# Optimization experiments

Hardware: AMD Instinct MI355X
Metric: run time of the kernel (lower is better)

## Reference

```python
import jax, jax.numpy as jnp
import numpy as np
from jax import lax

B, H, W = 2, 960, 1280
K = 1024            # max_keypoints
P = 256             # num_pairs (BAD descriptor dim)
NUM_SCALES = 3
DIFF_ITERS = 3
KAPPA = 0.05
TAU = 0.2           # explicit FED step size (stable < 0.25)
DET_THRESHOLD = 0.001
AKAZE_NMS = 5       # detector-internal NMS window
NMS_WIN = 2 * 3 + 1 # pipeline NMS window (nms_radius=3)
ORI_PATCH = 15
ORI_SIGMA = 2.5
SINK_ITERS = 20
EPSILON = 1.0
UNUSED_SCORE = 1.0
MAX_RADIUS = 5

def _conv(x, k):
    return lax.conv_general_dilated(x, k, (1, 1), 'SAME', dimension_numbers=('NCHW', 'OIHW', 'NCHW'))

_sob = np.array([[-1., 0., 1.], [-2., 0., 2.], [-1., 0., 1.]], np.float32) / 8.0
KX = jnp.asarray(_sob)[None, None]
KY = jnp.asarray(_sob.T)[None, None]
_d2 = np.array([[0., 0., 0.], [1., -2., 1.], [0., 0., 0.]], np.float32)
KXX = jnp.asarray(_d2)[None, None]
KYY = jnp.asarray(_d2.T)[None, None]

# Gaussian weighting kernel for orientation estimation
_c = np.arange(ORI_PATCH, dtype=np.float32) - (ORI_PATCH - 1) / 2.0
_gy, _gx = np.meshgrid(_c, _c, indexing='ij')
_g = np.exp(-(_gx ** 2 + _gy ** 2) / (2.0 * ORI_SIGMA ** 2))
GK = jnp.asarray((_g / _g.sum()).astype(np.float32))[None, None]

# Box-average kernel bank: one normalized box filter per radius 0..MAX_RADIUS
_bc = np.arange(-MAX_RADIUS, MAX_RADIUS + 1, dtype=np.float32)
_by, _bx = np.meshgrid(_bc, _bc, indexing='ij')
_rv = np.arange(MAX_RADIUS + 1, dtype=np.float32)[:, None, None]
_bm = ((np.abs(_by) <= _rv) & (np.abs(_bx) <= _rv)).astype(np.float32)
BOX_BANK = jnp.asarray((_bm / (2.0 * _rv + 1.0) ** 2)[:, None])  # [R+1,1,11,11]

def _shifts(a):
    p = jnp.pad(a, ((0, 0), (0, 0), (1, 1), (1, 1)), mode='edge')
    return p[:, :, :-2, 1:-1], p[:, :, 2:, 1:-1], p[:, :, 1:-1, :-2], p[:, :, 1:-1, 2:]

def _fed_step(L):
    # One explicit Perona-Malik (FED) nonlinear diffusion step
    Lx = _conv(L, KX); Ly = _conv(L, KY)
    g = 1.0 / (1.0 + (Lx * Lx + Ly * Ly) / (KAPPA * KAPPA))
    Ln, Ls, Lw, Le = _shifts(L)
    gn, gs, gw, ge = _shifts(g)
    flux = 0.5 * ((g + gn) * (Ln - L) + (g + gs) * (Ls - L) + (g + gw) * (Lw - L) + (g + ge) * (Le - L))
    return L + TAU * flux

def _maxpool(s, win):
    return lax.reduce_window(s, -jnp.inf, lax.max, (1, win, win), (1, 1, 1), 'SAME')

def _akaze(img):
    # Multi-scale FED diffusion -> Hessian determinant response + orientation map
    L = img
    resp = jnp.zeros((B, H, W), img.dtype)
    for _s in range(NUM_SCALES):
        for _i in range(DIFF_ITERS):
            L = _fed_step(L)
        Lxx = _conv(L, KXX); Lyy = _conv(L, KYY); Lxy = _conv(_conv(L, KX), KY)
        resp = jnp.maximum(resp, (Lxx * Lyy - Lxy * Lxy)[:, 0])
    resp = jnp.where(resp > DET_THRESHOLD, resp, 0.0)
    resp = resp * (resp >= _maxpool(resp, AKAZE_NMS) - 1e-7).astype(resp.dtype)
    gxs = _conv(_conv(img, KX), GK)[:, 0]
    gys = _conv(_conv(img, KY), GK)[:, 0]
    theta = jnp.arctan2(gys, gxs)  # [B,H,W]
    return resp, theta

def _select(resp):
    # Pipeline-level maxpool NMS + top-K selection, pad invalid with (-1,-1)
    mask = (resp >= _maxpool(resp, NMS_WIN) - 1e-7).astype(resp.dtype)
    s = resp * mask
    s = jnp.where(s > 0.0, s, 0.0)
    tk, idx = lax.top_k(s.reshape(B, -1), K)
    y = (idx // W).astype(jnp.float32)
    x = (idx % W).astype(jnp.float32)
    valid = (tk > 0.0).astype(jnp.float32)
    kpts = jnp.where(valid[..., None] > 0.5, jnp.stack([y, x], -1), -1.0)
    return kpts, tk * valid, valid

def _bad(img, kpts, theta, valid, offsets, radii, thresholds):
    # Orientation-aware BAD: box-averaged intensity differences at rotated pair offsets
    bank = _conv(img, BOX_BANK)  # [B,R+1,H,W]
    yc = jnp.clip(kpts[..., 0], 0.0, H - 1.0)
    xc = jnp.clip(kpts[..., 1], 0.0, W - 1.0)
    yi = jnp.round(yc).astype(jnp.int32); xi = jnp.round(xc).astype(jnp.int32)
    th = jax.vmap(lambda m, a, b: m[a, b])(theta, yi, xi)  # [B,K] nearest-sampled orientation
    c = jnp.cos(th)[..., None]; s = jnp.sin(th)[..., None]
    ox1, oy1, ox2, oy2 = offsets[:, 0], offsets[:, 1], offsets[:, 2], offsets[:, 3]
    px1 = xc[..., None] + c * ox1 - s * oy1
    py1 = yc[..., None] + s * ox1 + c * oy1
    px2 = xc[..., None] + c * ox2 - s * oy2
    py2 = yc[..., None] + s * ox2 + c * oy2
    rb = jnp.broadcast_to(radii[None, :], (K, P))
    def samp(px, py):
        xi_ = jnp.clip(jnp.round(px), 0, W - 1).astype(jnp.int32)
        yi_ = jnp.clip(jnp.round(py), 0, H - 1).astype(jnp.int32)
        return jax.vmap(lambda bk, a, b: bk[rb, a, b])(bank, yi_, xi_)  # [B,K,P]
    v = (samp(px1, py1) - samp(px2, py2)) - thresholds[None, None, :]
    v = v * valid[..., None]
    n = jnp.linalg.norm(v, axis=-1, keepdims=True)
    return v / (n + 1e-8)

def _sinkhorn(d1, d2):
    sq1 = jnp.sum(d1 * d1, -1); sq2 = jnp.sum(d2 * d2, -1)
    dist2 = sq1[:, :, None] + sq2[:, None, :] - 2.0 * jnp.einsum('bip,bjp->bij', d1, d2)
    dist = jnp.sqrt(jnp.maximum(dist2, 0.0) + 1e-12)
    Z = jnp.full((B, K + 1, K + 1), UNUSED_SCORE, d1.dtype)
    Z = Z.at[:, :K, :K].set(-dist) / EPSILON
    norm = -jnp.log(2.0 * K)
    log_mu = jnp.concatenate([jnp.zeros(K, Z.dtype), jnp.log(float(K)) * jnp.ones(1, Z.dtype)]) + norm
    log_nu = log_mu
    def body(carry, _):
        u, v = carry
        u = log_mu[None] - jax.nn.logsumexp(Z + v[:, None, :], axis=2)
        v = log_nu[None] - jax.nn.logsumexp(Z + u[:, :, None], axis=1)
        return (u, v), None
    (u, v), _ = lax.scan(body, (jnp.zeros((B, K + 1), Z.dtype), jnp.zeros((B, K + 1), Z.dtype)), None, length=SINK_ITERS)
    return jnp.exp(Z + u[:, :, None] + v[:, None, :] - norm)  # [B,K+1,K+1]

def _forward(img1, img2, offsets, thresholds, radii):
    r1, t1 = _akaze(img1)
    r2, t2 = _akaze(img2)
    k1, s1, v1 = _select(r1)
    k2, s2, v2 = _select(r2)
    d1 = _bad(img1, k1, t1, v1, offsets, radii, thresholds)
    d2 = _bad(img2, k2, t2, v2, offsets, radii, thresholds)
    probs = _sinkhorn(d1, d2)
    return k1, k2, probs

def setup_inputs():
    key = jax.random.key(0)
    k1, k2, k3, k4, k5 = jax.random.split(key, 5)
    img1 = jax.random.uniform(k1, (B, 1, H, W), jnp.float32)
    img2 = jax.random.uniform(k2, (B, 1, H, W), jnp.float32)
    offsets = jax.random.uniform(k3, (P, 4), jnp.float32, -16.0, 16.0)  # box_params - 16
    thresholds = 0.05 * jax.random.normal(k5, (P,), jnp.float32)
    radii = jax.random.randint(k4, (P,), 0, MAX_RADIUS + 1, jnp.int32)
    return {'img1': img1, 'img2': img2, 'offsets': offsets, 'thresholds': thresholds, 'radii': radii}

def reference(img1, img2, offsets, thresholds, radii):
    return _forward(img1, img2, offsets, thresholds, radii)
```

## Files before the change

kernel.cpp:

```cpp
#include <hip/hip_runtime.h>
#include <hip/hip_fp16.h>
#include <math.h>

typedef unsigned long long u64;
typedef unsigned int u32;

#define Hh 960
#define Ww 1280
#define Bb 2
#define Kk 1024
#define Pp 256
#define KP1 1025
#define NSEG 4
#define LISTCAP 131072
#define PR 28
#define PS 57
#define ZLD 1040
static const size_t ZB = (size_t)KP1*ZLD;

static const size_t HWp = (size_t)Hh * Ww;
static const size_t PLn = HWp * Bb;

#define TAUf 0.2f
#define NMS_EPS 1e-7f
#define DET_T 0.001f
#define NORMV (-7.6246189861593985f)
#define LOGKV (6.9314718055994531f)

__constant__ float WR[6] = {1.0f, 1.0f/9.0f, 1.0f/25.0f, 1.0f/49.0f, 1.0f/81.0f, 1.0f/121.0f};

__device__ __forceinline__ int imin(int a,int b){return a<b?a:b;}
__device__ __forceinline__ int imax(int a,int b){return a>b?a:b;}

__global__ __launch_bounds__(256) void fed_step(const float* __restrict__ src, float* __restrict__ dst){
  __shared__ float Lt[36][37];
  __shared__ float Gt[34][35];
  const int bx = blockIdx.x*32, by = blockIdx.y*32, b = blockIdx.z;
  const float* S = src + (size_t)b*HWp;
  float* D = dst + (size_t)b*HWp;
  const int t = threadIdx.y*32 + threadIdx.x;
  for (int i=t;i<36*36;i+=256){
    int ly=i/36, lx=i-ly*36;
    int gy=by+ly-2, gx=bx+lx-2;
    Lt[ly][lx] = (gy>=0 && gy<Hh && gx>=0 && gx<Ww) ? S[(size_t)gy*Ww+gx] : 0.0f;
  }
  __syncthreads();
  const float k2 = (float)(0.05*0.05);
  for (int i=t;i<34*34;i+=256){
    int ly=i/34, lx=i-ly*34;
    int Ly=ly+1, Lx=lx+1;
    float sx = (-Lt[Ly-1][Lx-1]+Lt[Ly-1][Lx+1]
                -2.0f*Lt[Ly][Lx-1]+2.0f*Lt[Ly][Lx+1]
                -Lt[Ly+1][Lx-1]+Lt[Ly+1][Lx+1])*0.125f;
    float sy = (-Lt[Ly-1][Lx-1]-2.0f*Lt[Ly-1][Lx]-Lt[Ly-1][Lx+1]
                +Lt[Ly+1][Lx-1]+2.0f*Lt[Ly+1][Lx]+Lt[Ly+1][Lx+1])*0.125f;
    Gt[ly][lx] = 1.0f/(1.0f + (sx*sx+sy*sy)/k2);
  }
  __syncthreads();
  for (int r=0;r<4;++r){
    int oy=threadIdx.y + r*8, ox=threadIdx.x;
    int gy=by+oy, gx=bx+ox;
    if (gy>=Hh || gx>=Ww) continue;
    int gyn=imax(gy-1,0), gys=imin(gy+1,Hh-1), gxw=imax(gx-1,0), gxe=imin(gx+1,Ww-1);
    float Lc=Lt[oy+2][ox+2];
    float Ln=Lt[gyn-by+2][ox+2];
    float Ls=Lt[gys-by+2][ox+2];
    float Lw=Lt[oy+2][gxw-bx+2];
    float Le=Lt[oy+2][gxe-bx+2];
    float gc=Gt[oy+1][ox+1];
    float gn=Gt[gyn-by+1][ox+1];
    float gs=Gt[gys-by+1][ox+1];
    float gw=Gt[oy+1][gxw-bx+1];
    float ge=Gt[oy+1][gxe-bx+1];
    float flux = 0.5f*((gc+gn)*(Ln-Lc) + (gc+gs)*(Ls-Lc) + (gc+gw)*(Lw-Lc) + (gc+ge)*(Le-Lc));
    D[(size_t)gy*Ww+gx] = Lc + TAUf*flux;
  }
}

__global__ __launch_bounds__(256) void response_kernel(const float* __restrict__ src, float* __restrict__ resp, int first){
  __shared__ float Lt[36][37];
  __shared__ float Sx[34][35];
  const int bx = blockIdx.x*32, by = blockIdx.y*32, b = blockIdx.z;
  const float* S = src + (size_t)b*HWp;
  float* R = resp + (size_t)b*HWp;
  const int t = threadIdx.y*32 + threadIdx.x;
  for (int i=t;i<36*36;i+=256){
    int ly=i/36, lx=i-ly*36;
    int gy=by+ly-2, gx=bx+lx-2;
    Lt[ly][lx] = (gy>=0 && gy<Hh && gx>=0 && gx<Ww) ? S[(size_t)gy*Ww+gx] : 0.0f;
  }
  __syncthreads();
  for (int i=t;i<34*34;i+=256){
    int ly=i/34, lx=i-ly*34;
    int gy=by+ly-1, gx=bx+lx-1;
    float v=0.0f;
    if (gy>=0 && gy<Hh && gx>=0 && gx<Ww){
      int Ly=ly+1, Lx=lx+1;
      v = (-Lt[Ly-1][Lx-1]+Lt[Ly-1][Lx+1]
           -2.0f*Lt[Ly][Lx-1]+2.0f*Lt[Ly][Lx+1]
           -Lt[Ly+1][Lx-1]+Lt[Ly+1][Lx+1])*0.125f;
    }
    Sx[ly][lx]=v;
  }
  __syncthreads();
  for (int r=0;r<4;++r){
    int oy=threadIdx.y + r*8, ox=threadIdx.x;
    int gy=by+oy, gx=bx+ox;
    if (gy>=Hh || gx>=Ww) continue;
    int Ly=oy+2, Lx=ox+2;
    float Lxx = Lt[Ly][Lx-1]-2.0f*Lt[Ly][Lx]+Lt[Ly][Lx+1];
    float Lyy = Lt[Ly-1][Lx]-2.0f*Lt[Ly][Lx]+Lt[Ly+1][Lx];
    int Sy=oy+1, Sxi=ox+1;
    float Lxy = (-Sx[Sy-1][Sxi-1]-2.0f*Sx[Sy-1][Sxi]-Sx[Sy-1][Sxi+1]
                 +Sx[Sy+1][Sxi-1]+2.0f*Sx[Sy+1][Sxi]+Sx[Sy+1][Sxi+1])*0.125f;
    float det = Lxx*Lyy - Lxy*Lxy;
    size_t id=(size_t)gy*Ww+gx;
    R[id] = first ? fmaxf(det,0.0f) : fmaxf(R[id], det);
  }
}

__global__ __launch_bounds__(256) void detect_compact(const float* __restrict__ resp,
                                                      u64* __restrict__ lists,
                                                      int* __restrict__ cnt, int segbase){
  const int TS=42;
  __shared__ float Tt[TS][TS+1];
  __shared__ float H5[TS][40];
  __shared__ float Ss[38][39];
  __shared__ u64 keys[1024];
  __shared__ int lcnt, gbase;
  const int bx = blockIdx.x*32, by = blockIdx.y*32, b = blockIdx.z;
  const float* S = resp + (size_t)b*HWp;
  const int t = threadIdx.y*32 + threadIdx.x;
  if (t==0) lcnt=0;
  for (int i=t;i<TS*TS;i+=256){
    int ly=i/TS, lx=i-ly*TS;
    int gy=by+ly-5, gx=bx+lx-5;
    float v = (gy>=0 && gy<Hh && gx>=0 && gx<Ww) ? S[(size_t)gy*Ww+gx] : 0.0f;
    Tt[ly][lx] = (v>DET_T) ? v : 0.0f;
  }
  __syncthreads();
  for (int i=t;i<42*38;i+=256){
    int y=i/38, x=i-(i/38)*38;
    float m=Tt[y][x];
    m=fmaxf(m,Tt[y][x+1]); m=fmaxf(m,Tt[y][x+2]);
    m=fmaxf(m,Tt[y][x+3]); m=fmaxf(m,Tt[y][x+4]);
    H5[y][x]=m;
  }
  __syncthreads();
  for (int i=t;i<38*38;i+=256){
    int y=i/38, x=i-(i/38)*38;
    float m=H5[y][x];
    m=fmaxf(m,H5[y+1][x]); m=fmaxf(m,H5[y+2][x]);
    m=fmaxf(m,H5[y+3][x]); m=fmaxf(m,H5[y+4][x]);
    float c=Tt[y+2][x+2];
    Ss[y][x]=(c>=m-NMS_EPS)?c:0.0f;
  }
  __syncthreads();
  const int seg=segbase+b;
  for (int r=0;r<4;++r){
    int oy=threadIdx.y + r*8, ox=threadIdx.x;
    int gy=by+oy, gx=bx+ox;
    bool pos=false; u64 key=0;
    if (gy<Hh && gx<Ww){
      float v=Ss[oy+3][ox+3];
      if (v>0.0f){
        float m=0.0f;
        #pragma unroll
        for(int dy=0;dy<7;dy++)
          #pragma unroll
          for(int dx=0;dx<7;dx++)
            m=fmaxf(m,Ss[oy+dy][ox+dx]);
        if (v>=m-NMS_EPS){
          u32 idx=(u32)(gy*Ww+gx);
          key=((u64)__float_as_uint(v)<<32)|(u64)(0xFFFFFFFFu-idx);
          pos=true;
        }
      }
    }
    u64 mask=__ballot(pos);
    if (mask){
      int lane=t&63;
      int leader=__ffsll((long long)mask)-1;
      int base=0;
      if (lane==leader) base=atomicAdd(&lcnt,__popcll(mask));
      base=__shfl(base,leader);
      if (pos){
        int rk=__popcll(mask & ((1ULL<<lane)-1ULL));
        keys[base+rk]=key;
      }
    }
  }
  __syncthreads();
  if (t==0 && lcnt>0) gbase=atomicAdd(&cnt[seg*64], lcnt);
  __syncthreads();
  int n=lcnt;
  for (int i=t;i<n;i+=256){
    int p=gbase+i;
    if (p<LISTCAP) lists[(size_t)seg*LISTCAP+p]=keys[i];
  }
}

__global__ __launch_bounds__(1024) void topk_one(const u64* __restrict__ lists, const int* __restrict__ cnt,
                                                 u64* __restrict__ selbuf, int* __restrict__ selcnt){
  const int seg=blockIdx.x, tid=threadIdx.x;
  __shared__ u32 h[256];
  __shared__ u32 scan[256];
  __shared__ int krem_s, ta_s, bsel, lbase;
  __shared__ u64 pfx_s;
  const int n=imin(cnt[seg*64],LISTCAP);
  const u64* L=lists+(size_t)seg*LISTCAP;
  if(tid==0){ krem_s=Kk; pfx_s=0ULL; ta_s=(n<=Kk)?1:0; lbase=0; }
  __syncthreads();
  u64 T=1ULL;
  if(!ta_s){
    for(int rd=0;rd<8;rd++){
      int shift=56-8*rd;
      u64 maskHi=(rd==0)?0ULL:(~0ULL<<(shift+8));
      u64 pfx=pfx_s;
      if(tid<256) h[tid]=0;
      __syncthreads();
      for(int i=tid;i<n;i+=1024){
        u64 k=L[i];
        if((k&maskHi)==pfx) atomicAdd(&h[(int)((k>>shift)&255ULL)],1u);
      }
      __syncthreads();
      if(tid<256) scan[tid]=h[tid];
      __syncthreads();
      for(int off=1;off<256;off<<=1){
        u32 v=0;
        if(tid<256 && tid+off<256) v=scan[tid+off];
        __syncthreads();
        if(tid<256) scan[tid]+=v;
        __syncthreads();
      }
      int kr=krem_s;
      if(tid<256){
        bool ge=(scan[tid]>=(u32)kr);
        bool geN=(tid<255)?(scan[tid+1]>=(u32)kr):false;
        if(ge && !geN) bsel=tid;
      }
      __syncthreads();
      if(tid==0){
        int b=bsel;
        int acc=(b<255)?(int)scan[b+1]:0;
        pfx_s |= ((u64)(u32)b)<<shift;
        krem_s = kr-acc;
      }
      __syncthreads();
    }
    T=pfx_s;
  }
  __syncthreads();
  for(int i0=0;i0<n;i0+=1024){
    int i=i0+tid;
    bool sel=false; u64 k=0;
    if(i<n){ k=L[i]; sel=(k>=T); }
    u64 mask=__ballot(sel);
    if(mask){
      int lane=tid&63;
      int leader=__ffsll((long long)mask)-1;
      int base=0;
      if(lane==leader) base=atomicAdd(&lbase,__popcll(mask));
      base=__shfl(base,leader);
      if(sel){
        int p=base+__popcll(mask & ((1ULL<<lane)-1ULL));
        if(p<Kk) selbuf[(size_t)seg*Kk+p]=k;
      }
    }
  }
  __syncthreads();
  if(tid==0) selcnt[seg*64]=imin(lbase,Kk);
}

__global__ __launch_bounds__(1024) void finalize_kernel(const u64* __restrict__ selbuf, const int* __restrict__ selcnt,
                                int* __restrict__ kyi, int* __restrict__ kxi, float* __restrict__ kval,
                                float* __restrict__ outp){
  int seg=blockIdx.x, tid=threadIdx.x;
  __shared__ u64 a[1024];
  int n=selcnt[seg*64]; if(n>Kk)n=Kk;
  a[tid]=(tid<n)?selbuf[(size_t)seg*Kk+tid]:0ULL;
  __syncthreads();
  for(int k=2;k<=1024;k<<=1){
    for(int j=k>>1;j>0;j>>=1){
      int ixj=tid^j;
      if(ixj>tid){
        u64 x=a[tid], y=a[ixj];
        bool desc=((tid&k)==0);
        if(desc ? (x<y) : (x>y)){ a[tid]=y; a[ixj]=x; }
      }
      __syncthreads();
    }
  }
  u64 key=a[tid];
  bool val=(key!=0ULL);
  u32 idx=0xFFFFFFFFu-(u32)(key&0xFFFFFFFFULL);
  int y= val ? (int)(idx/Ww) : 0;
  int x= val ? (int)(idx%Ww) : 0;
  int mi=seg*Kk+tid;
  kyi[mi]=y; kxi[mi]=x; kval[mi]= val?1.0f:0.0f;
  int imi=seg>>1, bb=seg&1;
  float* ko=outp + (size_t)imi*(Bb*Kk*2) + ((size_t)bb*Kk+tid)*2;
  ko[0]= val ? (float)y : -1.0f;
  ko[1]= val ? (float)x : -1.0f;
}

__global__ void init_weights(float* wn){
  if(threadIdx.x==0 && blockIdx.x==0){
    double w[15]; double S=0.0;
    for(int i=0;i<15;i++){ double c=(double)i-7.0; w[i]=exp(-(c*c)/(2.0*2.5*2.5)); S+=w[i]; }
    for(int i=0;i<15;i++) wn[i]=(float)(w[i]/S);
  }
}

__device__ __forceinline__ float ldz(const float* __restrict__ img,int y,int x){
  return (y>=0&&y<Hh&&x>=0&&x<Ww)?img[(size_t)y*Ww+x]:0.0f;
}

__global__ __launch_bounds__(64) void orient_kernel(const float* __restrict__ img1, const float* __restrict__ img2,
                              const int* __restrict__ kyi, const int* __restrict__ kxi,
                              const float* __restrict__ wn, float* __restrict__ kth){
  int seg=blockIdx.y, ki=blockIdx.x, lane=threadIdx.x;
  __shared__ float w15[15];
  if(lane<15) w15[lane]=wn[lane];
  __syncthreads();
  const float* img=(seg<2?img1:img2)+(size_t)(seg&1)*HWp;
  int mi=seg*Kk+ki;
  int yc=kyi[mi], xc=kxi[mi];
  float ax=0.0f, ay=0.0f;
  for(int tp=lane;tp<225;tp+=64){
    int du=tp/15-7, dv=tp-(tp/15)*15-7;
    int yy=yc+du, xx=xc+dv;
    if(yy<0||yy>=Hh||xx<0||xx>=Ww) continue;
    float p00=ldz(img,yy-1,xx-1), p01=ldz(img,yy-1,xx), p02=ldz(img,yy-1,xx+1);
    float p10=ldz(img,yy,xx-1),                          p12=ldz(img,yy,xx+1);
    float p20=ldz(img,yy+1,xx-1), p21=ldz(img,yy+1,xx), p22=ldz(img,yy+1,xx+1);
    float sx=(-p00+p02-2.0f*p10+2.0f*p12-p20+p22)*0.125f;
    float sy=(-p00-2.0f*p01-p02+p20+2.0f*p21+p22)*0.125f;
    float wgt=w15[du+7]*w15[dv+7];
    ax=fmaf(wgt,sx,ax); ay=fmaf(wgt,sy,ay);
  }
  for(int o=32;o;o>>=1){ ax+=__shfl_down(ax,o); ay+=__shfl_down(ay,o); }
  if(lane==0) kth[mi]=atan2f(ay,ax);
}

__global__ __launch_bounds__(256) void bad_kernel(const float* __restrict__ img1, const float* __restrict__ img2,
                           const float* __restrict__ offs, const float* __restrict__ thrv,
                           const int* __restrict__ rad,
                           const int* __restrict__ kyi, const int* __restrict__ kxi,
                           const float* __restrict__ kval, const float* __restrict__ kth,
                           float* __restrict__ d1, float* __restrict__ d2,
                           float* __restrict__ sq1, float* __restrict__ sq2){
  __shared__ float sat[PS+1][PS+2];
  __shared__ float sm[4];
  __shared__ float nsh;
  int seg=blockIdx.y, ki=blockIdx.x, p=threadIdx.x;
  const float* img=(seg<2?img1:img2)+(size_t)(seg&1)*HWp;
  int mi=seg*Kk+ki;
  int yci=kyi[mi], xci=kxi[mi];
  for (int i=p;i<PS+1;i+=256){ sat[0][i]=0.0f; sat[i][0]=0.0f; }
  if (p==0) sat[0][PS]=0.0f;
  for (int i=p;i<PS*PS;i+=256){
    int ly=i/PS, lx=i-ly*PS;
    int gy=yci-PR+ly, gx=xci-PR+lx;
    sat[ly+1][lx+1]=(gy>=0&&gy<Hh&&gx>=0&&gx<Ww)?img[(size_t)gy*Ww+gx]:0.0f;
  }
  __syncthreads();
  if (p<PS){
    float run=0.0f;
    for(int x=1;x<=PS;x++){ run+=sat[p+1][x]; sat[p+1][x]=run; }
  }
  __syncthreads();
  if (p<PS){
    float run=0.0f;
    for(int y=1;y<=PS;y++){ run+=sat[y][p+1]; sat[y][p+1]=run; }
  }
  __syncthreads();
  float yc=(float)yci, xc=(float)xci;
  float th=kth[mi];
  float c=cosf(th), s=sinf(th);
  float ox1=offs[p*4+0], oy1=offs[p*4+1], ox2=offs[p*4+2], oy2=offs[p*4+3];
  int r=rad[p];
  float w=WR[r];
  float px1=xc+c*ox1-s*oy1, py1=yc+s*ox1+c*oy1;
  float px2=xc+c*ox2-s*oy2, py2=yc+s*ox2+c*oy2;
  auto boxl=[&](float px,float py,int r_)->float{
    float rx=rintf(px), ry=rintf(py);
    int xi=(int)fminf(fmaxf(rx,0.0f),(float)(Ww-1));
    int yi=(int)fminf(fmaxf(ry,0.0f),(float)(Hh-1));
    int lx=xi-(xci-PR), ly=yi-(yci-PR);
    int y2=ly+r_+1, y1=ly-r_, x2=lx+r_+1, x1=lx-r_;
    return sat[y2][x2]-sat[y1][x2]-sat[y2][x1]+sat[y1][x1];
  };
  float s1=boxl(px1,py1,r)*w;
  float s2=boxl(px2,py2,r)*w;
  float v=(s1-s2-thrv[p])*kval[mi];
  float t=v*v;
  for(int o=32;o;o>>=1) t+=__shfl_down(t,o);
  if((p&63)==0) sm[p>>6]=t;
  __syncthreads();
  if(p==0) nsh=sqrtf(sm[0]+sm[1]+sm[2]+sm[3]);
  __syncthreads();
  float dv=v/(nsh+1e-8f);
  float* dd=(seg<2?d1:d2);
  dd[((size_t)(seg&1)*Kk+ki)*Pp+p]=dv;
  float t2=dv*dv;
  for(int o=32;o;o>>=1) t2+=__shfl_down(t2,o);
  __syncthreads();
  if((p&63)==0) sm[p>>6]=t2;
  __syncthreads();
  if(p==0){ float* sq=(seg<2?sq1:sq2); sq[(size_t)(seg&1)*Kk+ki]=sm[0]+sm[1]+sm[2]+sm[3]; }
}

__global__ __launch_bounds__(256) void dist_kernel(const float* __restrict__ d1, const float* __restrict__ d2,
                            const float* __restrict__ sq1, const float* __restrict__ sq2,
                            float* __restrict__ Zm, float* __restrict__ Zt){
  int b=blockIdx.z;
  int i0=blockIdx.y*64, j0=blockIdx.x*64;
  int tid=threadIdx.x;
  int tx=tid&15, ty=tid>>4;
  __shared__ float Ast[64][68], Bst[64][68];
  const float* D1=d1+(size_t)b*Kk*Pp;
  const float* D2=d2+(size_t)b*Kk*Pp;
  float acc[4][4]={};
  for(int p0=0;p0<Pp;p0+=64){
    for(int i=tid;i<64*16;i+=256){
      int row=i>>4, c4=(i&15)<<2;
      float4 va=*reinterpret_cast<const float4*>(&D1[(size_t)(i0+row)*Pp+p0+c4]);
      float4 vb=*reinterpret_cast<const float4*>(&D2[(size_t)(j0+row)*Pp+p0+c4]);
      Ast[c4+0][row]=va.x; Ast[c4+1][row]=va.y; Ast[c4+2][row]=va.z; Ast[c4+3][row]=va.w;
      Bst[c4+0][row]=vb.x; Bst[c4+1][row]=vb.y; Bst[c4+2][row]=vb.z; Bst[c4+3][row]=vb.w;
    }
    __syncthreads();
    #pragma unroll 8
    for(int kk=0;kk<64;++kk){
      float4 av=*reinterpret_cast<const float4*>(&Ast[kk][ty*4]);
      float4 bv=*reinterpret_cast<const float4*>(&Bst[kk][tx*4]);
      acc[0][0]=fmaf(av.x,bv.x,acc[0][0]); acc[0][1]=fmaf(av.x,bv.y,acc[0][1]);
      acc[0][2]=fmaf(av.x,bv.z,acc[0][2]); acc[0][3]=fmaf(av.x,bv.w,acc[0][3]);
      acc[1][0]=fmaf(av.y,bv.x,acc[1][0]); acc[1][1]=fmaf(av.y,bv.y,acc[1][1]);
      acc[1][2]=fmaf(av.y,bv.z,acc[1][2]); acc[1][3]=fmaf(av.y,bv.w,acc[1][3]);
      acc[2][0]=fmaf(av.z,bv.x,acc[2][0]); acc[2][1]=fmaf(av.z,bv.y,acc[2][1]);
      acc[2][2]=fmaf(av.z,bv.z,acc[2][2]); acc[2][3]=fmaf(av.z,bv.w,acc[2][3]);
      acc[3][0]=fmaf(av.w,bv.x,acc[3][0]); acc[3][1]=fmaf(av.w,bv.y,acc[3][1]);
      acc[3][2]=fmaf(av.w,bv.z,acc[3][2]); acc[3][3]=fmaf(av.w,bv.w,acc[3][3]);
    }
    __syncthreads();
  }
  int gi=i0+ty*4, gj=j0+tx*4;
  float si[4], sj[4];
  #pragma unroll
  for(int i=0;i<4;i++){ si[i]=sq1[b*Kk+gi+i]; sj[i]=sq2[b*Kk+gj+i]; }
  #pragma unroll
  for(int i=0;i<4;i++){
    #pragma unroll
    for(int j=0;j<4;j++){
      float dd=si[i]+sj[j]-2.0f*acc[i][j];
      float dist=sqrtf(fmaxf(dd,0.0f)+1e-12f);
      Zm[(size_t)b*ZB+(size_t)(gi+i)*ZLD+(gj+j)]=-dist;
      Zt[(size_t)b*ZB+(size_t)(gj+j)*ZLD+(gi+i)]=-dist;
    }
  }
}

__global__ void zborder_kernel(float* __restrict__ Zm, float* __restrict__ Zt){
  int i=blockIdx.x*256+threadIdx.x;
  if(i>=Bb*KP1) return;
  int b=i/KP1, j=i-(i/KP1)*KP1;
  size_t base=(size_t)b*ZB;
  Zm[base+(size_t)j*ZLD+Kk]=1.0f;
  Zm[base+(size_t)Kk*ZLD+j]=1.0f;
  Zt[base+(size_t)j*ZLD+Kk]=1.0f;
  Zt[base+(size_t)Kk*ZLD+j]=1.0f;
  for(int c=KP1;c<ZLD;c++){
    Zm[base+(size_t)j*ZLD+c]=-1.0e30f;
    Zt[base+(size_t)j*ZLD+c]=-1.0e30f;
  }
}

__global__ void expz_kernel(const float* __restrict__ Zm, const float* __restrict__ Zt,
                            __half* __restrict__ Em, __half* __restrict__ Et){
  size_t q=(size_t)blockIdx.x*256+threadIdx.x;
  const size_t tot4=(size_t)Bb*ZB/4;
  if(q>=2*tot4) return;
  const float* src=(q<tot4)?Zm:Zt;
  __half* dst=(q<tot4)?Em:Et;
  size_t j=(q<tot4)?q:q-tot4;
  float4 z=reinterpret_cast<const float4*>(src)[j];
  __half2 a=__floats2half2_rn(expf(z.x),expf(z.y));
  __half2 b=__floats2half2_rn(expf(z.z),expf(z.w));
  reinterpret_cast<__half2*>(dst)[2*j]=a;
  reinterpret_cast<__half2*>(dst)[2*j+1]=b;
}

__global__ void init_euv(float* __restrict__ euv, float* __restrict__ evv){
  int i=blockIdx.x*256+threadIdx.x;
  if(i>=Bb*ZLD) return;
  int j=i-(i/ZLD)*ZLD;
  evv[i]=(j<KP1)?1.0f:0.0f;
  euv[i]=0.0f;
}

struct H4{ __half2 a, b; };
__global__ __launch_bounds__(256) void sink_gemv(const __half* __restrict__ E,
        const float* __restrict__ evin, float* __restrict__ euout, float* __restrict__ uout){
  int row=blockIdx.x*4+(threadIdx.x>>6);
  if(row>=Bb*KP1) return;
  int b=row/KP1, i=row-b*KP1;
  int lane=threadIdx.x&63;
  const H4* e4=reinterpret_cast<const H4*>(E+((size_t)b*KP1+i)*ZLD);
  const float4* v4=reinterpret_cast<const float4*>(evin+(size_t)b*ZLD);
  float s=0.0f;
  for(int j=lane;j<ZLD/4;j+=64){
    H4 e=e4[j]; float4 v=v4[j];
    float2 ea=__half22float2(e.a), eb=__half22float2(e.b);
    s=fmaf(ea.x,v.x,s); s=fmaf(ea.y,v.y,s);
    s=fmaf(eb.x,v.z,s); s=fmaf(eb.y,v.w,s);
  }
  for(int o=32;o;o>>=1) s+=__shfl_down(s,o);
  if(lane==0){
    float lm,elm;
    if(i<Kk){ lm=NORMV; elm=4.8828125e-4f; }
    else    { lm=LOGKV+NORMV; elm=0.5f; }
    euout[(size_t)b*ZLD+i]=elm/s;
    uout [(size_t)b*ZLD+i]=lm-logf(s);
  }
}

__global__ void probs_kernel(const float* __restrict__ Zm, const float* __restrict__ uu,
                             const float* __restrict__ vv, float* __restrict__ outp){
  size_t i=(size_t)blockIdx.x*256+threadIdx.x;
  const size_t tot=(size_t)Bb*KP1*KP1;
  if(i>=tot) return;
  size_t b=i/((size_t)KP1*KP1);
  size_t rem=i-b*(size_t)KP1*KP1;
  int rr=(int)(rem/KP1), cc=(int)(rem-(size_t)(rem/KP1)*KP1);
  outp[i]=expf(Zm[b*ZB+(size_t)rr*ZLD+cc]+uu[b*ZLD+rr]+vv[b*ZLD+cc]-NORMV);
}

extern "C" void kernel_launch(void* const* d_in, const int* in_sizes, int n_in,
                              void* d_out, int out_size, void* d_ws, size_t ws_size,
                              hipStream_t stream) {
  (void)in_sizes; (void)n_in; (void)out_size;
  const float* img1=(const float*)d_in[0];
  const float* img2=(const float*)d_in[1];
  const float* offs=(const float*)d_in[2];
  const float* thrv=(const float*)d_in[3];
  const int*   rad =(const int*)d_in[4];
  float* out=(float*)d_out;

  const bool batched = ws_size >= ((size_t)72<<20);
  const int NP = batched ? 4 : 2;
  const size_t PB = HWp*(size_t)NP*4;

  char* wp=(char*)d_ws;
  auto carve=[&](size_t bytes)->char*{ char* p=wp; wp += (bytes+255)&~(size_t)255; return p; };
  float* r0  =(float*)carve(PB);
  float* r1  =(float*)carve(PB);
  float* resp=(float*)carve(PB);
  u64*  lists=(u64*)carve((size_t)NSEG*LISTCAP*8);
  char* stateblk = carve(8192);
  int* cnt     =(int*)(stateblk);
  int* selcnt  =(int*)(stateblk+1024);
  u64* selbuf  =(u64*)carve((size_t)NSEG*Kk*8);
  int* kyi     =(int*)carve((size_t)NSEG*Kk*4);
  int* kxi     =(int*)carve((size_t)NSEG*Kk*4);
  float* kval  =(float*)carve((size_t)NSEG*Kk*4);
  float* kth   =(float*)carve((size_t)NSEG*Kk*4);
  float* d1    =(float*)carve((size_t)Bb*Kk*Pp*4);
  float* d2    =(float*)carve((size_t)Bb*Kk*Pp*4);
  float* sq1   =(float*)carve((size_t)Bb*Kk*4);
  float* sq2   =(float*)carve((size_t)Bb*Kk*4);
  float* uvec  =(float*)carve((size_t)Bb*ZLD*4);
  float* vvec  =(float*)carve((size_t)Bb*ZLD*4);
  float* euvec =(float*)carve((size_t)Bb*ZLD*4);
  float* evvec =(float*)carve((size_t)Bb*ZLD*4);
  float* wn    =(float*)carve(64);

  const size_t EBYTES = ((size_t)Bb*ZB*2 + 255)&~(size_t)255;
  __half* Em=(__half*)resp;
  __half* Et=(__half*)((char*)resp + EBYTES);

  hipMemsetAsync(stateblk, 0, 8192, stream);
  init_weights<<<1,32,0,stream>>>(wn);

  dim3 TB(32,8);
  if (batched){
    dim3 TG(Ww/32, Hh/32, 4);
    hipMemcpyAsync(r0,       img1, PLn*4, hipMemcpyDeviceToDevice, stream);
    hipMemcpyAsync(r0+2*HWp, img2, PLn*4, hipMemcpyDeviceToDevice, stream);
    float* cur=r0; float* oth=r1;
    for(int st=1; st<=9; ++st){
      fed_step<<<TG,TB,0,stream>>>(cur, oth);
      float* tp=cur; cur=oth; oth=tp;
      if(st%3==0) response_kernel<<<TG,TB,0,stream>>>(cur, resp, st==3);
    }
    detect_compact<<<TG,TB,0,stream>>>(resp, lists, cnt, 0);
  } else {
    dim3 TG(Ww/32, Hh/32, Bb);
    for(int im=0; im<2; ++im){
      const float* srcimg = (im==0)? img1 : img2;
      hipMemcpyAsync(r0, srcimg, PLn*4, hipMemcpyDeviceToDevice, stream);
      float* cur=r0; float* oth=r1;
      for(int st=1; st<=9; ++st){
        fed_step<<<TG,TB,0,stream>>>(cur, oth);
        float* tp=cur; cur=oth; oth=tp;
        if(st%3==0) response_kernel<<<TG,TB,0,stream>>>(cur, resp, st==3);
      }
      detect_compact<<<TG,TB,0,stream>>>(resp, lists, cnt, im*2);
    }
  }

  topk_one<<<dim3(NSEG),dim3(1024),0,stream>>>(lists, cnt, selbuf, selcnt);
  finalize_kernel<<<NSEG,1024,0,stream>>>(selbuf, selcnt, kyi, kxi, kval, out);
  orient_kernel<<<dim3(Kk,NSEG),dim3(64),0,stream>>>(img1, img2, kyi, kxi, wn, kth);
  bad_kernel<<<dim3(Kk,NSEG),dim3(256),0,stream>>>(img1, img2, offs, thrv, rad,
                                                   kyi, kxi, kval, kth, d1, d2, sq1, sq2);

  float* Zm=r0; float* Zt=r1;
  dist_kernel<<<dim3(16,16,Bb),dim3(256),0,stream>>>(d1,d2,sq1,sq2,Zm,Zt);
  zborder_kernel<<<dim3((Bb*KP1+255)/256),dim3(256),0,stream>>>(Zm,Zt);
  {
    size_t tot4=(size_t)Bb*ZB/4;
    expz_kernel<<<dim3((u32)((2*tot4+255)/256)),dim3(256),0,stream>>>(Zm,Zt,Em,Et);
  }
  init_euv<<<dim3((Bb*ZLD+255)/256),dim3(256),0,stream>>>(euvec,evvec);
  for(int it=0; it<20; ++it){
    sink_gemv<<<dim3((Bb*KP1+3)/4),dim3(256),0,stream>>>(Em, evvec, euvec, uvec);
    sink_gemv<<<dim3((Bb*KP1+3)/4),dim3(256),0,stream>>>(Et, euvec, evvec, vvec);
  }
  size_t tot=(size_t)Bb*KP1*KP1;
  probs_kernel<<<dim3((u32)((tot+255)/256)),dim3(256),0,stream>>>(Zm, uvec, vvec, out + (size_t)2*Bb*Kk*2);
}
```

Baseline: 628.2 us.

## Split single-block radix top-k into multi-block histogram, compact, finish and gather

Replaces the one-block-per-segment 8-pass radix select with a multi-block 16-bit histogram over the top key bits. A decide kernel then picks the boundary bucket, the keys in that bucket are compacted to a small candidate buffer, and the remaining 6 radix passes run over those candidates in LDS. The final gather runs across many blocks. This spreads the memory-bound scans over the whole GPU and cuts repeated full-list passes, at the cost of more launches, a 1 MB histogram memset, and a higher workspace threshold for the batched path.

```diff
diff --git a/kernel.cpp b/kernel.cpp
--- a/kernel.cpp
+++ b/kernel.cpp
@@ -16,6 +16,7 @@
 #define PR 28
 #define PS 57
 #define ZLD 1040
+#define CANDCAP 8192
 static const size_t ZB = (size_t)KP1*ZLD;
 
 static const size_t HWp = (size_t)Hh * Ww;
@@ -200,27 +201,106 @@
   }
 }
 
-__global__ __launch_bounds__(1024) void topk_one(const u64* __restrict__ lists, const int* __restrict__ cnt,
-                                                 u64* __restrict__ selbuf, int* __restrict__ selcnt){
-  const int seg=blockIdx.x, tid=threadIdx.x;
-  __shared__ u32 h[256];
-  __shared__ u32 scan[256];
-  __shared__ int krem_s, ta_s, bsel, lbase;
-  __shared__ u64 pfx_s;
-  const int n=imin(cnt[seg*64],LISTCAP);
+__global__ __launch_bounds__(256) void topk_hist16(const u64* __restrict__ lists, const int* __restrict__ cnt,
+                                                   u32* __restrict__ h16){
+  int seg=blockIdx.y;
+  int n=imin(cnt[seg*64],LISTCAP);
   const u64* L=lists+(size_t)seg*LISTCAP;
-  if(tid==0){ krem_s=Kk; pfx_s=0ULL; ta_s=(n<=Kk)?1:0; lbase=0; }
-  __syncthreads();
-  u64 T=1ULL;
-  if(!ta_s){
-    for(int rd=0;rd<8;rd++){
-      int shift=56-8*rd;
-      u64 maskHi=(rd==0)?0ULL:(~0ULL<<(shift+8));
-      u64 pfx=pfx_s;
+  u32* H=h16+(size_t)seg*65536;
+  for(int i=blockIdx.x*256+threadIdx.x;i<n;i+=gridDim.x*256){
+    u32 b=(u32)(L[i]>>48);
+    atomicAdd(&H[b],1u);
+  }
+}
+
+__global__ __launch_bounds__(1024) void topk_decide16(const u32* __restrict__ h16, const int* __restrict__ cnt,
+                                                      int* __restrict__ b16o, int* __restrict__ krem16,
+                                                      int* __restrict__ takeAll, u64* __restrict__ Tf){
+  int seg=blockIdx.x, tid=threadIdx.x;
+  __shared__ u32 sc[1024];
+  const u32* H=h16+(size_t)seg*65536;
+  int n=imin(cnt[seg*64],LISTCAP);
+  if(n<=Kk){
+    if(tid==0){ takeAll[seg]=1; Tf[seg]=1ULL; b16o[seg]=-1; }
+    return;
+  }
+  u32 csum=0;
+  u32 hl[  64];
+  #pragma unroll 8
+  for(int j=0;j<64;j++){ hl[j]=H[tid*64+j]; csum+=hl[j]; }
+  sc[tid]=csum;
+  __syncthreads();
+  for(int off=1;off<1024;off<<=1){
+    u32 v=(tid+off<1024)?sc[tid+off]:0u;
+    __syncthreads();
+    sc[tid]+=v;
+    __syncthreads();
+  }
+  u32 nxt=(tid<1023)?sc[tid+1]:0u;
+  if(sc[tid]>=(u32)Kk && nxt<(u32)Kk){
+    u32 run=nxt;
+    for(int j=63;j>=0;j--){
+      u32 c=hl[j];
+      run+=c;
+      if(run>=(u32)Kk){
+        b16o[seg]=tid*64+j;
+        krem16[seg]=Kk-(int)(run-c);
+        takeAll[seg]=0;
+        break;
+      }
+    }
+  }
+}
+
+__global__ __launch_bounds__(256) void topk_compact(const u64* __restrict__ lists, const int* __restrict__ cnt,
+                                                    const int* __restrict__ b16o, const int* __restrict__ takeAll,
+                                                    u64* __restrict__ candbuf, int* __restrict__ candcnt){
+  int seg=blockIdx.y;
+  if(takeAll[seg]) return;
+  int n=imin(cnt[seg*64],LISTCAP);
+  const u64* L=lists+(size_t)seg*LISTCAP;
+  u32 b16=(u32)b16o[seg];
+  for(int i0=blockIdx.x*256;i0<n;i0+=gridDim.x*256){
+    int i=i0+threadIdx.x;
+    bool sel=false; u64 k=0;
+    if(i<n){ k=L[i]; sel=((u32)(k>>48)==b16); }
+    u64 mask=__ballot(sel);
+    if(mask){
+      int lane=threadIdx.x&63;
+      int leader=__ffsll((long long)mask)-1;
+      int base=0;
+      if(lane==leader) base=atomicAdd(&candcnt[seg*64],__popcll(mask));
+      base=__shfl(base,leader);
+      if(sel){
+        int p=base+__popcll(mask & ((1ULL<<lane)-1ULL));
+        if(p<CANDCAP) candbuf[(size_t)seg*CANDCAP+p]=k;
+      }
+    }
+  }
+}
+
+__global__ __launch_bounds__(1024) void topk_finish(const u64* __restrict__ lists, const int* __restrict__ cnt,
+                                                    const u64* __restrict__ candbuf, const int* __restrict__ candcnt,
+                                                    const int* __restrict__ b16o, const int* __restrict__ krem16,
+                                                    const int* __restrict__ takeAll, u64* __restrict__ Tf){
+  int seg=blockIdx.x, tid=threadIdx.x;
+  if(takeAll[seg]) return;
+  __shared__ u64 cands[CANDCAP];
+  __shared__ u32 h[256], scan[256];
+  __shared__ int bsel;
+  int cc=candcnt[seg*64];
+  u64 pfx=((u64)(u32)b16o[seg])<<48;
+  int kr=krem16[seg];
+  if(cc<=CANDCAP){
+    for(int i=tid;i<cc;i+=1024) cands[i]=candbuf[(size_t)seg*CANDCAP+i];
+    __syncthreads();
+    for(int rd=0;rd<6;rd++){
+      int shift=40-8*rd;
+      u64 maskHi=~0ULL<<(shift+8);
       if(tid<256) h[tid]=0;
       __syncthreads();
-      for(int i=tid;i<n;i+=1024){
-        u64 k=L[i];
+      for(int i=tid;i<cc;i+=1024){
+        u64 k=cands[i];
         if((k&maskHi)==pfx) atomicAdd(&h[(int)((k>>shift)&255ULL)],1u);
       }
       __syncthreads();
@@ -233,34 +313,73 @@
         if(tid<256) scan[tid]+=v;
         __syncthreads();
       }
-      int kr=krem_s;
       if(tid<256){
         bool ge=(scan[tid]>=(u32)kr);
         bool geN=(tid<255)?(scan[tid+1]>=(u32)kr):false;
         if(ge && !geN) bsel=tid;
       }
       __syncthreads();
-      if(tid==0){
-        int b=bsel;
-        int acc=(b<255)?(int)scan[b+1]:0;
-        pfx_s |= ((u64)(u32)b)<<shift;
-        krem_s = kr-acc;
-      }
-      __syncthreads();
-    }
-    T=pfx_s;
-  }
-  __syncthreads();
-  for(int i0=0;i0<n;i0+=1024){
-    int i=i0+tid;
+      int b=bsel;
+      int acc=(b<255)?(int)scan[b+1]:0;
+      pfx |= ((u64)(u32)b)<<shift;
+      kr -= acc;
+      __syncthreads();
+    }
+  } else {
+    int n=imin(cnt[seg*64],LISTCAP);
+    const u64* L=lists+(size_t)seg*LISTCAP;
+    for(int rd=0;rd<6;rd++){
+      int shift=40-8*rd;
+      u64 maskHi=~0ULL<<(shift+8);
+      if(tid<256) h[tid]=0;
+      __syncthreads();
+      for(int i=tid;i<n;i+=1024){
+        u64 k=L[i];
+        if((k&maskHi)==pfx) atomicAdd(&h[(int)((k>>shift)&255ULL)],1u);
+      }
+      __syncthreads();
+      if(tid<256) scan[tid]=h[tid];
+      __syncthreads();
+      for(int off=1;off<256;off<<=1){
+        u32 v=0;
+        if(tid<256 && tid+off<256) v=scan[tid+off];
+        __syncthreads();
+        if(tid<256) scan[tid]+=v;
+        __syncthreads();
+      }
+      if(tid<256){
+        bool ge=(scan[tid]>=(u32)kr);
+        bool geN=(tid<255)?(scan[tid+1]>=(u32)kr):false;
+        if(ge && !geN) bsel=tid;
+      }
+      __syncthreads();
+      int b=bsel;
+      int acc=(b<255)?(int)scan[b+1]:0;
+      pfx |= ((u64)(u32)b)<<shift;
+      kr -= acc;
+      __syncthreads();
+    }
+  }
+  if(tid==0) Tf[seg]=pfx;
+}
+
+__global__ __launch_bounds__(256) void topk_gather(const u64* __restrict__ lists, const int* __restrict__ cnt,
+                                                   const u64* __restrict__ Tf, u64* __restrict__ selbuf,
+                                                   int* __restrict__ selcnt){
+  int seg=blockIdx.y;
+  int n=imin(cnt[seg*64],LISTCAP);
+  u64 T=Tf[seg];
+  const u64* L=lists+(size_t)seg*LISTCAP;
+  for(int i0=blockIdx.x*256;i0<n;i0+=gridDim.x*256){
+    int i=i0+threadIdx.x;
     bool sel=false; u64 k=0;
     if(i<n){ k=L[i]; sel=(k>=T); }
     u64 mask=__ballot(sel);
     if(mask){
-      int lane=tid&63;
+      int lane=threadIdx.x&63;
       int leader=__ffsll((long long)mask)-1;
       int base=0;
-      if(lane==leader) base=atomicAdd(&lbase,__popcll(mask));
+      if(lane==leader) base=atomicAdd(&selcnt[seg*64],__popcll(mask));
       base=__shfl(base,leader);
       if(sel){
         int p=base+__popcll(mask & ((1ULL<<lane)-1ULL));
@@ -268,8 +387,6 @@
       }
     }
   }
-  __syncthreads();
-  if(tid==0) selcnt[seg*64]=imin(lbase,Kk);
 }
 
 __global__ __launch_bounds__(1024) void finalize_kernel(const u64* __restrict__ selbuf, const int* __restrict__ selcnt,
@@ -548,7 +665,7 @@
   const int*   rad =(const int*)d_in[4];
   float* out=(float*)d_out;
 
-  const bool batched = ws_size >= ((size_t)72<<20);
+  const bool batched = ws_size >= ((size_t)80<<20);
   const int NP = batched ? 4 : 2;
   const size_t PB = HWp*(size_t)NP*4;
 
@@ -561,6 +678,13 @@
   char* stateblk = carve(8192);
   int* cnt     =(int*)(stateblk);
   int* selcnt  =(int*)(stateblk+1024);
+  int* b16o    =(int*)(stateblk+2048);
+  int* krem16  =(int*)(stateblk+2112);
+  int* takeAll =(int*)(stateblk+2176);
+  u64* Tf      =(u64*)(stateblk+2240);
+  int* candcnt =(int*)(stateblk+4096);
+  u32* h16     =(u32*)carve((size_t)NSEG*65536*4);
+  u64* candbuf =(u64*)carve((size_t)NSEG*CANDCAP*8);
   u64* selbuf  =(u64*)carve((size_t)NSEG*Kk*8);
   int* kyi     =(int*)carve((size_t)NSEG*Kk*4);
   int* kxi     =(int*)carve((size_t)NSEG*Kk*4);
@@ -581,6 +705,7 @@
   __half* Et=(__half*)((char*)resp + EBYTES);
 
   hipMemsetAsync(stateblk, 0, 8192, stream);
+  hipMemsetAsync(h16, 0, (size_t)NSEG*65536*4, stream);
   init_weights<<<1,32,0,stream>>>(wn);
 
   dim3 TB(32,8);
@@ -610,7 +735,11 @@
     }
   }
 
-  topk_one<<<dim3(NSEG),dim3(1024),0,stream>>>(lists, cnt, selbuf, selcnt);
+  topk_hist16 <<<dim3(32,NSEG),dim3(256),0,stream>>>(lists, cnt, h16);
+  topk_decide16<<<dim3(NSEG),dim3(1024),0,stream>>>(h16, cnt, b16o, krem16, takeAll, Tf);
+  topk_compact<<<dim3(32,NSEG),dim3(256),0,stream>>>(lists, cnt, b16o, takeAll, candbuf, candcnt);
+  topk_finish <<<dim3(NSEG),dim3(1024),0,stream>>>(lists, cnt, candbuf, candcnt, b16o, krem16, takeAll, Tf);
+  topk_gather <<<dim3(32,NSEG),dim3(256),0,stream>>>(lists, cnt, Tf, selbuf, selcnt);
   finalize_kernel<<<NSEG,1024,0,stream>>>(selbuf, selcnt, kyi, kxi, kval, out);
   orient_kernel<<<dim3(Kk,NSEG),dim3(64),0,stream>>>(img1, img2, kyi, kxi, wn, kth);
   bad_kernel<<<dim3(Kk,NSEG),dim3(256),0,stream>>>(img1, img2, offs, thrv, rad,
```

After: 628.7 us. Within noise of the previous version (+0.1%).
